# Performance work log

Measured on AMD Instinct MI355X. Metric: run time of the kernel, lower is better.

## Reference

```python
import jax, jax.numpy as jnp
import numpy as np

BATCH = 16384
MAZE_LEN = 3844  # 31*31*4
P = 0.0          # init kwarg p (default)
CLAMP_MIN = float(np.exp(-90.0))

# is_f(maze,row,col,tile) = maze[4*col + 124*row + tile]
IDX_A = 4 * 1 + 124 * 0 + 2    # is_f(maze, 0, 1, 2)  -> 6
IDX_B = 4 * 29 + 124 * 30 + 3  # is_f(maze, 30, 29, 3) -> 3839

def _chain_indices():
    idx = []
    for i in range(31):
        idx.append(124 * i + 1)    # is_f(maze, i, 0, 1)
        idx.append(124 * i + 121)  # is_f(maze, i, 30, 1)
    for i in range(28):
        idx.append(4 * (i + 2) + 1)   # is_f(maze, 0, i+2, 1)
        idx.append(4 * i + 3721)      # is_f(maze, 30, i, 1)
    return np.asarray(idx, dtype=np.int32)

CHAIN_IDX = jnp.asarray(_chain_indices())  # [118]

def _and_f(x, y, p):
    # Hamacher fuzzy AND: x*y / (p + (1-p)*(x+y-x*y)).
    # (original has a 0/0 guard only for x==y==p==0; inputs are in (0,1) here)
    denom = p + (1.0 - p) * (x + y - x * y)
    return x * y / denom

def setup_inputs() -> dict:
    key = jax.random.key(0)
    maze = jax.random.uniform(key, (BATCH, MAZE_LEN), dtype=jnp.float32)
    return {"maze": maze}

def reference(maze) -> jnp.ndarray:
    p = P
    # initial AND of the two special tiles
    result = _and_f(maze[:, IDX_A], maze[:, IDX_B], p)  # [B]
    vals = maze[:, CHAIN_IDX]  # [B, 118] gathered chain operands
    def step(carry, v):  # carry: [B], v: [B]
        return _and_f(carry, v, p), None
    result, _ = jax.lax.scan(step, result, vals.T)  # sequential per-element, vectorized over batch
    clamped = jnp.clip(result, CLAMP_MIN)
    return jnp.mean(-jnp.log(clamped))
```

## Files before the change

### kernel.cpp

```cpp
#include <hip/hip_runtime.h>
#include <math.h>

#define BATCH    16384
#define MAZE_LEN 3844
#define NCHUNK   961
#define ROWS_PER_BLOCK 8
#define NBLK1    (BATCH / ROWS_PER_BLOCK)
#define NTERMS   120.0f


struct WTab { float w[1024][4]; };

static constexpr WTab make_w() {
    WTab t{};
    int W[MAZE_LEN] = {};
    W[4 * 1 + 124 * 0 + 2]  += 1;
    W[4 * 29 + 124 * 30 + 3] += 1;
    for (int i = 0; i < 31; ++i) { W[124 * i + 1] += 1; W[124 * i + 121] += 1; }
    for (int i = 0; i < 28; ++i) { W[4 * (i + 2) + 1] += 1; W[4 * i + 3721] += 1; }
    for (int c = 0; c < NCHUNK; ++c)
        for (int j = 0; j < 4; ++j) t.w[c][j] = (float)W[4 * c + j];
    return t;
}

__constant__ WTab c_w = make_w();

__global__ __launch_bounds__(256) void fuzzy_rows(
        const float* __restrict__ maze, float* __restrict__ partial) {
    const int tid  = threadIdx.x;
    const int lane = tid & 63;
    const int wave = tid >> 6;

    float4 w[4], B[4];
    int off[4];
    #pragma unroll
    for (int k = 0; k < 4; ++k) {
        const int c  = tid + (k << 8);
        const int cc = (c < NCHUNK) ? c : (NCHUNK - 1);
        off[k] = cc << 2;
        const int wc = (c < NCHUNK) ? c : 1023;
        w[k] = *(const float4*)&c_w.w[wc][0];
        B[k].x = (w[k].x == 0.0f) ? 1e30f : 0.0f;
        B[k].y = (w[k].y == 0.0f) ? 1e30f : 0.0f;
        B[k].z = (w[k].z == 0.0f) ? 1e30f : 0.0f;
        B[k].w = (w[k].w == 0.0f) ? 1e30f : 0.0f;
    }

    __shared__ float s_part[4][ROWS_PER_BLOCK];
    __shared__ float s_fin[ROWS_PER_BLOCK];

    const float* rp = maze + (size_t)blockIdx.x * ROWS_PER_BLOCK * MAZE_LEN;

    for (int r = 0; r < ROWS_PER_BLOCK; ++r, rp += MAZE_LEN) {
        float a0 = 0.0f, a1 = 0.0f, a2 = 0.0f, a3 = 0.0f;
        #pragma unroll
        for (int k = 0; k < 4; ++k) {
            const float4 v = *(const float4*)(rp + off[k]);
            a0 = fmaf(w[k].x, __builtin_amdgcn_rcpf(v.x + B[k].x), a0);
            a1 = fmaf(w[k].y, __builtin_amdgcn_rcpf(v.y + B[k].y), a1);
            a2 = fmaf(w[k].z, __builtin_amdgcn_rcpf(v.z + B[k].z), a2);
            a3 = fmaf(w[k].w, __builtin_amdgcn_rcpf(v.w + B[k].w), a3);
        }
        float p = (a0 + a1) + (a2 + a3);
        #pragma unroll
        for (int o = 32; o > 0; o >>= 1) p += __shfl_xor(p, o, 64);
        if (lane == 0) s_part[wave][r] = p;
    }
    __syncthreads();

    if (tid < ROWS_PER_BLOCK) {
        const float S = s_part[0][tid] + s_part[1][tid]
                      + s_part[2][tid] + s_part[3][tid] - NTERMS;
        s_fin[tid] = fminf(log1pf(S), 90.0f);
    }
    __syncthreads();

    if (tid == 0) {
        float t = 0.0f;
        #pragma unroll
        for (int r = 0; r < ROWS_PER_BLOCK; ++r) t += s_fin[r];
        partial[blockIdx.x] = t;
    }
}

__global__ __launch_bounds__(256) void reduce_partials(
        const float* __restrict__ partial, float* __restrict__ out) {
    float t = 0.0f;
    #pragma unroll
    for (int i = 0; i < NBLK1 / 256; ++i)
        t += partial[threadIdx.x + (i << 8)];

    #pragma unroll
    for (int o = 32; o > 0; o >>= 1) t += __shfl_xor(t, o, 64);

    __shared__ float s_part[4];
    if ((threadIdx.x & 63) == 0) s_part[threadIdx.x >> 6] = t;
    __syncthreads();

    if (threadIdx.x == 0)
        out[0] = (s_part[0] + s_part[1] + s_part[2] + s_part[3])
                 * (1.0f / (float)BATCH);
}

extern "C" void kernel_launch(void* const* d_in, const int* in_sizes, int n_in,
                              void* d_out, int out_size, void* d_ws, size_t ws_size,
                              hipStream_t stream) {
    const float* maze = (const float*)d_in[0];
    float* out  = (float*)d_out;
    float* part = (float*)d_ws;

    fuzzy_rows<<<dim3(NBLK1), dim3(256), 0, stream>>>(maze, part);
    reduce_partials<<<dim3(1), dim3(256), 0, stream>>>(part, out);
}
```

Before: 339.8 us.

## Process four rows per block with all loads issued together for memory parallelism

```diff
diff --git a/kernel.cpp b/kernel.cpp
--- a/kernel.cpp
+++ b/kernel.cpp
@@ -4,8 +4,8 @@
 #define BATCH    16384
 #define MAZE_LEN 3844
 #define NCHUNK   961
-#define ROWS_PER_BLOCK 8
-#define NBLK1    (BATCH / ROWS_PER_BLOCK)
+#define RPB      4
+#define NBLK1    (BATCH / RPB)
 #define NTERMS   120.0f
 
 
@@ -25,62 +25,86 @@
 
 __constant__ WTab c_w = make_w();
 
-__global__ __launch_bounds__(256) void fuzzy_rows(
+__global__ __launch_bounds__(256, 8) void fuzzy_rows(
         const float* __restrict__ maze, float* __restrict__ partial) {
     const int tid  = threadIdx.x;
     const int lane = tid & 63;
     const int wave = tid >> 6;
 
-    float4 w[4], B[4];
-    int off[4];
+    const float* r0 = maze + (size_t)blockIdx.x * (RPB * MAZE_LEN);
+    const float* r1 = r0 + MAZE_LEN;
+    const float* r2 = r1 + MAZE_LEN;
+    const float* r3 = r2 + MAZE_LEN;
+
+    float a0 = 0.0f, a1 = 0.0f, a2 = 0.0f, a3 = 0.0f;
+
     #pragma unroll
     for (int k = 0; k < 4; ++k) {
         const int c  = tid + (k << 8);
         const int cc = (c < NCHUNK) ? c : (NCHUNK - 1);
-        off[k] = cc << 2;
         const int wc = (c < NCHUNK) ? c : 1023;
-        w[k] = *(const float4*)&c_w.w[wc][0];
-        B[k].x = (w[k].x == 0.0f) ? 1e30f : 0.0f;
-        B[k].y = (w[k].y == 0.0f) ? 1e30f : 0.0f;
-        B[k].z = (w[k].z == 0.0f) ? 1e30f : 0.0f;
-        B[k].w = (w[k].w == 0.0f) ? 1e30f : 0.0f;
+        const int o  = cc << 2;
+
+        const float4 v0 = *(const float4*)(r0 + o);
+        const float4 v1 = *(const float4*)(r1 + o);
+        const float4 v2 = *(const float4*)(r2 + o);
+        const float4 v3 = *(const float4*)(r3 + o);
+        const float4 w  = *(const float4*)&c_w.w[wc][0];
+
+        float4 b;
+        b.x = (w.x == 0.0f) ? 1e30f : 0.0f;
+        b.y = (w.y == 0.0f) ? 1e30f : 0.0f;
+        b.z = (w.z == 0.0f) ? 1e30f : 0.0f;
+        b.w = (w.w == 0.0f) ? 1e30f : 0.0f;
+
+        a0 = fmaf(w.x, __builtin_amdgcn_rcpf(v0.x + b.x), a0);
+        a0 = fmaf(w.y, __builtin_amdgcn_rcpf(v0.y + b.y), a0);
+        a0 = fmaf(w.z, __builtin_amdgcn_rcpf(v0.z + b.z), a0);
+        a0 = fmaf(w.w, __builtin_amdgcn_rcpf(v0.w + b.w), a0);
+
+        a1 = fmaf(w.x, __builtin_amdgcn_rcpf(v1.x + b.x), a1);
+        a1 = fmaf(w.y, __builtin_amdgcn_rcpf(v1.y + b.y), a1);
+        a1 = fmaf(w.z, __builtin_amdgcn_rcpf(v1.z + b.z), a1);
+        a1 = fmaf(w.w, __builtin_amdgcn_rcpf(v1.w + b.w), a1);
+
+        a2 = fmaf(w.x, __builtin_amdgcn_rcpf(v2.x + b.x), a2);
+        a2 = fmaf(w.y, __builtin_amdgcn_rcpf(v2.y + b.y), a2);
+        a2 = fmaf(w.z, __builtin_amdgcn_rcpf(v2.z + b.z), a2);
+        a2 = fmaf(w.w, __builtin_amdgcn_rcpf(v2.w + b.w), a2);
+
+        a3 = fmaf(w.x, __builtin_amdgcn_rcpf(v3.x + b.x), a3);
+        a3 = fmaf(w.y, __builtin_amdgcn_rcpf(v3.y + b.y), a3);
+        a3 = fmaf(w.z, __builtin_amdgcn_rcpf(v3.z + b.z), a3);
+        a3 = fmaf(w.w, __builtin_amdgcn_rcpf(v3.w + b.w), a3);
     }
 
-    __shared__ float s_part[4][ROWS_PER_BLOCK];
-    __shared__ float s_fin[ROWS_PER_BLOCK];
+    #pragma unroll
+    for (int off = 32; off > 0; off >>= 1) {
+        a0 += __shfl_xor(a0, off, 64);
+        a1 += __shfl_xor(a1, off, 64);
+        a2 += __shfl_xor(a2, off, 64);
+        a3 += __shfl_xor(a3, off, 64);
+    }
 
-    const float* rp = maze + (size_t)blockIdx.x * ROWS_PER_BLOCK * MAZE_LEN;
-
-    for (int r = 0; r < ROWS_PER_BLOCK; ++r, rp += MAZE_LEN) {
-        float a0 = 0.0f, a1 = 0.0f, a2 = 0.0f, a3 = 0.0f;
-        #pragma unroll
-        for (int k = 0; k < 4; ++k) {
-            const float4 v = *(const float4*)(rp + off[k]);
-            a0 = fmaf(w[k].x, __builtin_amdgcn_rcpf(v.x + B[k].x), a0);
-            a1 = fmaf(w[k].y, __builtin_amdgcn_rcpf(v.y + B[k].y), a1);
-            a2 = fmaf(w[k].z, __builtin_amdgcn_rcpf(v.z + B[k].z), a2);
-            a3 = fmaf(w[k].w, __builtin_amdgcn_rcpf(v.w + B[k].w), a3);
-        }
-        float p = (a0 + a1) + (a2 + a3);
-        #pragma unroll
-        for (int o = 32; o > 0; o >>= 1) p += __shfl_xor(p, o, 64);
-        if (lane == 0) s_part[wave][r] = p;
+    __shared__ float s_part[4][RPB];
+    __shared__ float s_fin[RPB];
+    if (lane == 0) {
+        s_part[wave][0] = a0;
+        s_part[wave][1] = a1;
+        s_part[wave][2] = a2;
+        s_part[wave][3] = a3;
     }
     __syncthreads();
 
-    if (tid < ROWS_PER_BLOCK) {
+    if (tid < RPB) {
         const float S = s_part[0][tid] + s_part[1][tid]
                       + s_part[2][tid] + s_part[3][tid] - NTERMS;
         s_fin[tid] = fminf(log1pf(S), 90.0f);
     }
     __syncthreads();
 
-    if (tid == 0) {
-        float t = 0.0f;
-        #pragma unroll
-        for (int r = 0; r < ROWS_PER_BLOCK; ++r) t += s_fin[r];
-        partial[blockIdx.x] = t;
-    }
+    if (tid == 0)
+        partial[blockIdx.x] = s_fin[0] + s_fin[1] + s_fin[2] + s_fin[3];
 }
 
 __global__ __launch_bounds__(256) void reduce_partials(
```

Measured after the change: 346.1 us. Within noise of the previous version (+1.9%).
